# Performance work log

Hardware: AMD Instinct MI355X
Metric: run time of the kernel (lower is better)

The kernel has to match this reference:

```python
import jax, jax.numpy as jnp
import numpy as np

N = 100000
LEAKY_SLOPE = 0.2


def gat_conv(x, W, att_src, att_dst, b, src, dst, num_nodes):
    """PyG-style GATConv (concat=True). x:[N,Fin], W:[Fin,H*C], att_*:[1,H,C], b:[H*C]."""
    H, C = att_src.shape[1], att_src.shape[2]
    h = (x @ W).reshape(num_nodes, H, C)                      # [N,H,C]
    a_src = jnp.sum(h * att_src, axis=-1)                     # [N,H]
    a_dst = jnp.sum(h * att_dst, axis=-1)                     # [N,H]
    e = jax.nn.leaky_relu(a_src[src] + a_dst[dst], LEAKY_SLOPE)  # [E,H]
    # segment softmax over destination neighborhoods
    m = jax.ops.segment_max(e, dst, num_segments=num_nodes)   # [N,H]
    m = jnp.where(jnp.isfinite(m), m, 0.0)
    ex = jnp.exp(e - m[dst])                                  # [E,H]
    s = jax.ops.segment_sum(ex, dst, num_segments=num_nodes)  # [N,H]
    alpha = ex / (s[dst] + 1e-16)                             # [E,H]
    msg = h[src] * alpha[:, :, None]                          # [E,H,C]
    out = jax.ops.segment_sum(msg, dst, num_segments=num_nodes)  # [N,H,C]
    return out.reshape(num_nodes, H * C) + b


def setup_inputs() -> dict:
    key = jax.random.key(0)
    ks = jax.random.split(key, 8)
    F_in, H, C, n_cls = 256, 4, 32, 16
    E = 1_600_000
    x = jax.random.normal(ks[0], (N, F_in), dtype=jnp.float32)
    edge_index = jax.random.randint(ks[1], (2, E), 0, N, dtype=jnp.int64)
    sc1 = 1.0 / np.sqrt(F_in)
    sc2 = 1.0 / np.sqrt(H * C)
    return {
        "x": x,
        "edge_index": edge_index,
        "W1": jax.random.normal(ks[2], (F_in, H * C), dtype=jnp.float32) * sc1,
        "att_src1": jax.random.normal(ks[3], (1, H, C), dtype=jnp.float32) * sc2,
        "att_dst1": jax.random.normal(ks[4], (1, H, C), dtype=jnp.float32) * sc2,
        "b1": jnp.zeros((H * C,), dtype=jnp.float32),
        "W2": jax.random.normal(ks[5], (H * C, n_cls), dtype=jnp.float32) * sc2,
        "att_src2": jax.random.normal(ks[6], (1, 1, n_cls), dtype=jnp.float32) * 0.25,
        "att_dst2": jax.random.normal(ks[7], (1, 1, n_cls), dtype=jnp.float32) * 0.25,
        "b2": jnp.zeros((n_cls,), dtype=jnp.float32),
    }


def reference(x, edge_index, W1, att_src1, att_dst1, b1, W2, att_src2, att_dst2, b2):
    # add self-loops (PyG GATConv default)
    loop = jnp.arange(N, dtype=edge_index.dtype)
    src = jnp.concatenate([edge_index[0], loop])
    dst = jnp.concatenate([edge_index[1], loop])
    # eval mode: dropout(p=0.6) is identity
    h = gat_conv(x, W1, att_src1, att_dst1, b1, src, dst, N)
    h = jax.nn.elu(h)
    out = gat_conv(h, W2, att_src2, att_dst2, b2, src, dst, N)
    return out
```

## Files before the change

### kernel.cpp

```cpp
#include <hip/hip_runtime.h>
#include <hip/hip_fp16.h>
#include <cfloat>
#include <cmath>

#define LEAKY 0.2f

typedef _Float16 half8 __attribute__((ext_vector_type(8)));
typedef float f32x4 __attribute__((ext_vector_type(4)));

__device__ __forceinline__ void edge_sd(const int* __restrict__ ei, int e, int E, int& s, int& d) {
    if (e < E) { s = ei[e]; d = ei[E + e]; }
    else       { s = e - E; d = e - E; }
}

__global__ void hist_k(const int* __restrict__ ei, int E, int ET,
                       int* __restrict__ cnt, int* __restrict__ rank) {
    int e = blockIdx.x * 256 + threadIdx.x;
    if (e >= ET) return;
    int d = (e < E) ? ei[E + e] : e - E;
    rank[e] = atomicAdd(&cnt[d], 1);
}

__device__ __forceinline__ int wave_incl_scan(int x, int lane) {
#pragma unroll
    for (int off = 1; off < 64; off <<= 1) {
        int y = __shfl_up(x, off);
        if (lane >= off) x += y;
    }
    return x;
}

__global__ __launch_bounds__(1024) void scan_blk_k(const int* __restrict__ cnt,
                                                   int* __restrict__ rowptr,
                                                   int* __restrict__ part, int Nn) {
    __shared__ int wsum[16];
    const int t = threadIdx.x, lane = t & 63, w = t >> 6;
    const int i = blockIdx.x * 1024 + t;
    int v = (i < Nn) ? cnt[i] : 0;
    int sc = wave_incl_scan(v, lane);
    if (lane == 63) wsum[w] = sc;
    __syncthreads();
    if (w == 0 && lane < 16) {
        int x = wsum[lane];
#pragma unroll
        for (int off = 1; off < 16; off <<= 1) {
            int y = __shfl_up(x, off);
            if (lane >= off) x += y;
        }
        wsum[lane] = x;
    }
    __syncthreads();
    int excl = sc - v + (w ? wsum[w - 1] : 0);
    if (i < Nn) rowptr[i] = excl;
    if (t == 1023) part[blockIdx.x] = wsum[15];
}

__global__ __launch_bounds__(128) void scan_part_k(int* __restrict__ part, int nb) {
    __shared__ int sm[128];
    int t = threadIdx.x;
    int v = (t < nb) ? part[t] : 0;
    sm[t] = v; __syncthreads();
    for (int off = 1; off < 128; off <<= 1) {
        int add = (t >= off) ? sm[t - off] : 0;
        __syncthreads();
        sm[t] += add;
        __syncthreads();
    }
    if (t < nb) part[t] = sm[t] - v;
}

__global__ __launch_bounds__(1024) void scan_add_k(int* __restrict__ rowptr,
                                                   const int* __restrict__ part,
                                                   int Nn, int ET) {
    int i = blockIdx.x * 1024 + threadIdx.x;
    if (i < Nn) rowptr[i] += part[blockIdx.x];
    if (i == 0) rowptr[Nn] = ET;
}

__global__ void scatter_k(const int* __restrict__ ei, int E, int ET,
                          const int* __restrict__ rowptr, const int* __restrict__ rank,
                          int* __restrict__ srcs) {
    int e = blockIdx.x * 256 + threadIdx.x;
    if (e >= ET) return;
    int s, d; edge_sd(ei, e, E, s, d);
    srcs[rowptr[d] + rank[e]] = s;
}

__global__ void wpack1_k(const float* __restrict__ W1, _Float16* __restrict__ Wpk) {
    int g = blockIdx.x * 256 + threadIdx.x;
    if (g >= 4096) return;
    int t = g >> 9, s = (g >> 6) & 7, l = g & 63;
    int krow = s * 32 + ((l >> 4) << 3);
    int col = t * 16 + (l & 15);
    half8 v;
#pragma unroll
    for (int j = 0; j < 8; ++j) v[j] = (_Float16)W1[(size_t)(krow + j) * 128 + col];
    *(half8*)&Wpk[(size_t)g * 8] = v;
}

__global__ __launch_bounds__(512) void gemm1_k(const float* __restrict__ x,
                                               const _Float16* __restrict__ Wpk,
                                               _Float16* __restrict__ h1, int Mt) {
    __shared__ __align__(16) _Float16 xs[32 * 256];
    const int t = threadIdx.x;
    const int l = t & 63;
    const int w = t >> 6;
    const int mstr = w >> 2;
    const int npair = w & 3;

    half8 bf0[8], bf1[8];
#pragma unroll
    for (int s = 0; s < 8; ++s) {
        bf0[s] = *(const half8*)&Wpk[(size_t)(((npair * 2 + 0) * 8 + s) * 64 + l) * 8];
        bf1[s] = *(const half8*)&Wpk[(size_t)(((npair * 2 + 1) * 8 + s) * 64 + l) * 8];
    }

    const int r = t >> 4;
    const int kc = t & 15;
    const int swz = (r & 7) << 4;
    const int arow = mstr * 16 + (l & 15);
    const int aswz = (arow & 7) << 4;
    const int abase = arow * 256;

    for (int mt = blockIdx.x; mt < Mt; mt += gridDim.x) {
        const int mBase = mt * 32;
        const float4* xrow = (const float4*)(x + (size_t)(mBase + r) * 256);
#pragma unroll
        for (int i = 0; i < 4; ++i) {
            float4 v = xrow[kc + i * 16];
            union { _Float16 h[4]; uint2 u; } cv;
            cv.h[0] = (_Float16)v.x; cv.h[1] = (_Float16)v.y;
            cv.h[2] = (_Float16)v.z; cv.h[3] = (_Float16)v.w;
            int kb = kc * 8 + i * 128;
            *(uint2*)&xs[r * 256 + ((kb ^ swz) >> 1)] = cv.u;
        }
        __syncthreads();
        f32x4 acc0 = {0.f, 0.f, 0.f, 0.f}, acc1 = {0.f, 0.f, 0.f, 0.f};
#pragma unroll
        for (int s = 0; s < 8; ++s) {
            int kb = s * 64 + ((l >> 4) << 4);
            half8 a = *(const half8*)&xs[abase + ((kb ^ aswz) >> 1)];
            acc0 = __builtin_amdgcn_mfma_f32_16x16x32_f16(a, bf0[s], acc0, 0, 0, 0);
            acc1 = __builtin_amdgcn_mfma_f32_16x16x32_f16(a, bf1[s], acc1, 0, 0, 0);
        }
        const int drow = mBase + mstr * 16 + ((l >> 4) << 2);
        const int dcol = npair * 32 + (l & 15);
#pragma unroll
        for (int rr = 0; rr < 4; ++rr) {
            h1[(size_t)(drow + rr) * 128 + dcol]      = (_Float16)acc0[rr];
            h1[(size_t)(drow + rr) * 128 + dcol + 16] = (_Float16)acc1[rr];
        }
        __syncthreads();
    }
}

__global__ void acoef1_k(const __half* __restrict__ h1, const float* __restrict__ att_s,
                         const float* __restrict__ att_d, float* __restrict__ a1s,
                         float* __restrict__ a1d, int Nn) {
    int g = blockIdx.x * 256 + threadIdx.x;
    if (g >= Nn * 4) return;
    int node = g >> 2, head = g & 3;
    const __half2* hp = (const __half2*)(h1 + (size_t)node * 128 + head * 32);
    const float* as = att_s + head * 32;
    const float* ad = att_d + head * 32;
    float s = 0.0f, d = 0.0f;
#pragma unroll
    for (int c = 0; c < 16; ++c) {
        float2 v = __half22float2(hp[c]);
        s += v.x * as[2 * c] + v.y * as[2 * c + 1];
        d += v.x * ad[2 * c] + v.y * ad[2 * c + 1];
    }
    a1s[g] = s; a1d[g] = d;
}

__global__ __launch_bounds__(256) void agg1_k(const int* __restrict__ rowptr,
                                              const int* __restrict__ srcs,
                                              const float* __restrict__ a1s,
                                              const float* __restrict__ a1d,
                                              const __half* __restrict__ h1,
                                              const float* __restrict__ b1,
                                              const float* __restrict__ W2,
                                              const float* __restrict__ att_s2,
                                              const float* __restrict__ att_d2,
                                              __half* __restrict__ h2,
                                              float* __restrict__ a2s,
                                              float* __restrict__ a2d, int Nn) {
    __shared__ int   s_s[4][64];
    __shared__ float s_al[4][64][4];
    __shared__ float rowb[4][128];
    __shared__ float w2s[128 * 16];
    const int wv = threadIdx.x >> 6;
    const int lane = threadIdx.x & 63;
    const int n = blockIdx.x * 4 + wv;

    for (int i4 = threadIdx.x; i4 < 512; i4 += 256)
        *(float4*)&w2s[i4 * 4] = *(const float4*)&W2[i4 * 4];

    if (n < Nn) {
        const int beg = rowptr[n], end = rowptr[n + 1];
        const int cnt = end - beg;
        const float4 ad4 = ((const float4*)a1d)[n];

        int e = beg + lane;
        bool val = e < end;
        int sv = val ? srcs[e] : 0;
        float4 a = ((const float4*)a1s)[sv];
        float v0 = a.x + ad4.x, v1 = a.y + ad4.y, v2 = a.z + ad4.z, v3 = a.w + ad4.w;
        v0 = fmaxf(v0, LEAKY * v0); v1 = fmaxf(v1, LEAKY * v1);
        v2 = fmaxf(v2, LEAKY * v2); v3 = fmaxf(v3, LEAKY * v3);
        float al0 = val ? __expf(v0) : 0.0f, al1 = val ? __expf(v1) : 0.0f;
        float al2 = val ? __expf(v2) : 0.0f, al3 = val ? __expf(v3) : 0.0f;
        float t0 = al0, t1 = al1, t2 = al2, t3 = al3;
        for (int base = beg + 64; base < end; base += 64) {
            int ee = base + lane; bool vv = ee < end;
            int ss = vv ? srcs[ee] : 0;
            float4 aa = ((const float4*)a1s)[ss];
            float w0 = aa.x + ad4.x, w1 = aa.y + ad4.y, w2v = aa.z + ad4.z, w3 = aa.w + ad4.w;
            w0 = fmaxf(w0, LEAKY * w0); w1 = fmaxf(w1, LEAKY * w1);
            w2v = fmaxf(w2v, LEAKY * w2v); w3 = fmaxf(w3, LEAKY * w3);
            if (vv) { t0 += __expf(w0); t1 += __expf(w1); t2 += __expf(w2v); t3 += __expf(w3); }
        }
#pragma unroll
        for (int off = 1; off < 64; off <<= 1) {
            t0 += __shfl_xor(t0, off); t1 += __shfl_xor(t1, off);
            t2 += __shfl_xor(t2, off); t3 += __shfl_xor(t3, off);
        }
        const float i0 = 1.0f / (t0 + 1e-16f), i1 = 1.0f / (t1 + 1e-16f);
        const float i2 = 1.0f / (t2 + 1e-16f), i3 = 1.0f / (t3 + 1e-16f);

        const int hc = lane >> 4;
        float2 acc = make_float2(0.0f, 0.0f);
        const size_t lo = 2 * lane;

        s_s[wv][lane] = sv;
        s_al[wv][lane][0] = al0 * i0; s_al[wv][lane][1] = al1 * i1;
        s_al[wv][lane][2] = al2 * i2; s_al[wv][lane][3] = al3 * i3;
        int wcnt = cnt < 64 ? cnt : 64;
        int ko = 0;
        for (; ko + 4 <= wcnt; ko += 4) {
            int s0 = s_s[wv][ko+0], s1 = s_s[wv][ko+1];
            int s2 = s_s[wv][ko+2], s3 = s_s[wv][ko+3];
            float p0 = s_al[wv][ko+0][hc], p1 = s_al[wv][ko+1][hc];
            float p2 = s_al[wv][ko+2][hc], p3 = s_al[wv][ko+3][hc];
            float2 g0 = __half22float2(*(const __half2*)&h1[(size_t)s0 * 128 + lo]);
            float2 g1 = __half22float2(*(const __half2*)&h1[(size_t)s1 * 128 + lo]);
            float2 g2 = __half22float2(*(const __half2*)&h1[(size_t)s2 * 128 + lo]);
            float2 g3 = __half22float2(*(const __half2*)&h1[(size_t)s3 * 128 + lo]);
            acc.x = fmaf(p0, g0.x, acc.x); acc.y = fmaf(p0, g0.y, acc.y);
            acc.x = fmaf(p1, g1.x, acc.x); acc.y = fmaf(p1, g1.y, acc.y);
            acc.x = fmaf(p2, g2.x, acc.x); acc.y = fmaf(p2, g2.y, acc.y);
            acc.x = fmaf(p3, g3.x, acc.x); acc.y = fmaf(p3, g3.y, acc.y);
        }
        for (; ko < wcnt; ++ko) {
            int s = s_s[wv][ko];
            float p = s_al[wv][ko][hc];
            float2 g = __half22float2(*(const __half2*)&h1[(size_t)s * 128 + lo]);
            acc.x = fmaf(p, g.x, acc.x); acc.y = fmaf(p, g.y, acc.y);
        }
        for (int base = beg + 64; base < end; base += 64) {
            int ee = base + lane; bool vv = ee < end;
            int ss = vv ? srcs[ee] : 0;
            float4 aa = ((const float4*)a1s)[ss];
            float w0 = aa.x + ad4.x, w1 = aa.y + ad4.y, w2v = aa.z + ad4.z, w3 = aa.w + ad4.w;
            w0 = fmaxf(w0, LEAKY * w0); w1 = fmaxf(w1, LEAKY * w1);
            w2v = fmaxf(w2v, LEAKY * w2v); w3 = fmaxf(w3, LEAKY * w3);
            s_s[wv][lane] = ss;
            s_al[wv][lane][0] = vv ? __expf(w0) * i0 : 0.0f;
            s_al[wv][lane][1] = vv ? __expf(w1) * i1 : 0.0f;
            s_al[wv][lane][2] = vv ? __expf(w2v) * i2 : 0.0f;
            s_al[wv][lane][3] = vv ? __expf(w3) * i3 : 0.0f;
            int wc = end - base; if (wc > 64) wc = 64;
            for (int k2 = 0; k2 < wc; ++k2) {
                int s = s_s[wv][k2];
                float p = s_al[wv][k2][hc];
                float2 g = __half22float2(*(const __half2*)&h1[(size_t)s * 128 + lo]);
                acc.x = fmaf(p, g.x, acc.x); acc.y = fmaf(p, g.y, acc.y);
            }
        }
        float2 bb = *(const float2*)&b1[2 * lane];
        float ox = acc.x + bb.x, oy = acc.y + bb.y;
        ox = ox > 0.0f ? ox : expm1f(ox);
        oy = oy > 0.0f ? oy : expm1f(oy);
        rowb[wv][2 * lane] = ox;
        rowb[wv][2 * lane + 1] = oy;
    }
    __syncthreads();
    if (n >= Nn) return;

    const int q = lane >> 4, j = lane & 15;
    const float* rb = rowb[wv];
    float part = 0.0f;
#pragma unroll
    for (int kk = 0; kk < 32; ++kk) {
        int k = kk * 4 + q;
        part = fmaf(rb[k], w2s[k * 16 + j], part);
    }
    part += __shfl_xor(part, 16);
    part += __shfl_xor(part, 32);
    float vs = part * att_s2[j];
    float vd = part * att_d2[j];
#pragma unroll
    for (int off = 1; off < 16; off <<= 1) {
        vs += __shfl_xor(vs, off);
        vd += __shfl_xor(vd, off);
    }
    if (lane < 16) h2[(size_t)n * 16 + j] = __float2half(part);
    if (lane == 0) { a2s[n] = vs; a2d[n] = vd; }
}

__global__ __launch_bounds__(256) void agg2_k(const int* __restrict__ rowptr,
                                              const int* __restrict__ srcs,
                                              const float* __restrict__ a2s,
                                              const float* __restrict__ a2d,
                                              const __half* __restrict__ h2,
                                              const float* __restrict__ b2,
                                              float* __restrict__ dout, int Nn) {
    __shared__ int   s_s[4][64];
    __shared__ float s_al[4][64];
    const int wv = threadIdx.x >> 6;
    const int lane = threadIdx.x & 63;
    const int n = blockIdx.x * 4 + wv;
    if (n >= Nn) return;
    const int beg = rowptr[n], end = rowptr[n + 1];
    const int cnt = end - beg;
    const float adn = a2d[n];

    int e = beg + lane;
    bool val = e < end;
    int sv = val ? srcs[e] : 0;
    float av = a2s[sv] + adn;
    av = fmaxf(av, LEAKY * av);
    float al = val ? __expf(av) : 0.0f;
    float ss = al;
    for (int base = beg + 64; base < end; base += 64) {
        int ee = base + lane; bool vv = ee < end;
        float aw = a2s[vv ? srcs[ee] : 0] + adn;
        aw = fmaxf(aw, LEAKY * aw);
        if (vv) ss += __expf(aw);
    }
#pragma unroll
    for (int off = 1; off < 64; off <<= 1) ss += __shfl_xor(ss, off);
    const float sinv = 1.0f / (ss + 1e-16f);

    const int eg = lane >> 4, j = lane & 15;
    float acc = 0.0f;
    s_s[wv][lane] = sv;
    s_al[wv][lane] = al * sinv;
    int wcnt = cnt < 64 ? cnt : 64;
    int ko = eg;
    for (; ko + 4 < wcnt; ko += 8) {
        int s0 = s_s[wv][ko], s1 = s_s[wv][ko + 4];
        float p0 = s_al[wv][ko], p1 = s_al[wv][ko + 4];
        float g0 = __half2float(h2[(size_t)s0 * 16 + j]);
        float g1 = __half2float(h2[(size_t)s1 * 16 + j]);
        acc = fmaf(p0, g0, acc);
        acc = fmaf(p1, g1, acc);
    }
    for (; ko < wcnt; ko += 4) {
        acc = fmaf(s_al[wv][ko], __half2float(h2[(size_t)s_s[wv][ko] * 16 + j]), acc);
    }
    for (int base = beg + 64; base < end; base += 64) {
        int ee = base + lane; bool vv = ee < end;
        int sn = vv ? srcs[ee] : 0;
        float aw = a2s[sn] + adn;
        aw = fmaxf(aw, LEAKY * aw);
        s_s[wv][lane] = sn;
        s_al[wv][lane] = vv ? __expf(aw) * sinv : 0.0f;
        int wc = end - base; if (wc > 64) wc = 64;
        for (int k2 = eg; k2 < wc; k2 += 4) {
            acc = fmaf(s_al[wv][k2], __half2float(h2[(size_t)s_s[wv][k2] * 16 + j]), acc);
        }
    }
    acc += __shfl_xor(acc, 16);
    acc += __shfl_xor(acc, 32);
    if (lane < 16) dout[(size_t)n * 16 + j] = acc + b2[j];
}

extern "C" void kernel_launch(void* const* d_in, const int* in_sizes, int n_in,
                              void* d_out, int out_size, void* d_ws, size_t ws_size,
                              hipStream_t stream) {
    const float* x      = (const float*)d_in[0];
    const int*   ei     = (const int*)d_in[1];
    const float* W1     = (const float*)d_in[2];
    const float* att_s1 = (const float*)d_in[3];
    const float* att_d1 = (const float*)d_in[4];
    const float* b1     = (const float*)d_in[5];
    const float* W2     = (const float*)d_in[6];
    const float* att_s2 = (const float*)d_in[7];
    const float* att_d2 = (const float*)d_in[8];
    const float* b2     = (const float*)d_in[9];
    float* dout = (float*)d_out;

    const int Nn = in_sizes[0] / 256;
    const int E  = in_sizes[1] / 2;
    const int ET = E + Nn;

    char* p = (char*)d_ws;
    auto alloc = [&](size_t bytes) { char* r = p; p += (bytes + 255) & ~(size_t)255; return r; };
    _Float16* h1  = (_Float16*)alloc((size_t)Nn * 128 * 2);
    __half* h2    = (__half*)alloc((size_t)Nn * 16 * 2);
    _Float16* Wpk = (_Float16*)alloc(4096 * 8 * 2);
    float* a1s    = (float*)alloc((size_t)Nn * 4 * 4);
    float* a1d    = (float*)alloc((size_t)Nn * 4 * 4);
    float* a2s    = (float*)alloc((size_t)Nn * 4);
    float* a2d    = (float*)alloc((size_t)Nn * 4);
    int* rowptr   = (int*)alloc((size_t)(Nn + 1) * 4);
    int* cnt      = (int*)alloc((size_t)Nn * 4);
    int* rank     = (int*)alloc((size_t)ET * 4);
    int* part     = (int*)alloc(128 * 4);
    int* srcs     = (int*)alloc((size_t)ET * 4);

    const int nbScan = (Nn + 1023) / 1024;

    hipMemsetAsync(cnt, 0, (size_t)Nn * 4, stream);
    hist_k<<<dim3((ET + 255) / 256), dim3(256), 0, stream>>>(ei, E, ET, cnt, rank);
    scan_blk_k<<<dim3(nbScan), dim3(1024), 0, stream>>>(cnt, rowptr, part, Nn);
    scan_part_k<<<dim3(1), dim3(128), 0, stream>>>(part, nbScan);
    scan_add_k<<<dim3(nbScan), dim3(1024), 0, stream>>>(rowptr, part, Nn, ET);
    scatter_k<<<dim3((ET + 255) / 256), dim3(256), 0, stream>>>(ei, E, ET, rowptr, rank, srcs);
    wpack1_k<<<dim3(16), dim3(256), 0, stream>>>(W1, Wpk);
    gemm1_k<<<dim3(512), dim3(512), 0, stream>>>(x, Wpk, h1, Nn / 32);
    acoef1_k<<<dim3((Nn * 4 + 255) / 256), dim3(256), 0, stream>>>((const __half*)h1, att_s1, att_d1, a1s, a1d, Nn);
    agg1_k<<<dim3((Nn + 3) / 4), dim3(256), 0, stream>>>(rowptr, srcs, a1s, a1d,
                                                         (const __half*)h1, b1,
                                                         W2, att_s2, att_d2,
                                                         h2, a2s, a2d, Nn);
    agg2_k<<<dim3((Nn + 3) / 4), dim3(256), 0, stream>>>(rowptr, srcs, a2s, a2d, h2, b2, dout, Nn);
}
```

Baseline: 290.1 us.

## Fuse attention coefficient computation into GEMM epilogue and vectorize CSR build kernels

Removes the separate acoef1 kernel by computing per-head source and destination attention dot products in the GEMM epilogue. Each 16-lane group reduces its columns with xor shuffles and one lane writes the result. The histogram and scatter kernels now process four edges per thread with int4 loads, cutting thread count and improving load width. This assumes E is divisible by 4 and 16-byte alignment of the edge arrays, and the attention coefficients now come from fp32 accumulators rather than fp16-rounded h1.

```diff
diff --git a/kernel.cpp b/kernel.cpp
--- a/kernel.cpp
+++ b/kernel.cpp
@@ -13,12 +13,22 @@
     else       { s = e - E; d = e - E; }
 }
 
-__global__ void hist_k(const int* __restrict__ ei, int E, int ET,
+__global__ void hist_k(const int* __restrict__ ei, int E, int Nn,
                        int* __restrict__ cnt, int* __restrict__ rank) {
-    int e = blockIdx.x * 256 + threadIdx.x;
-    if (e >= ET) return;
-    int d = (e < E) ? ei[E + e] : e - E;
-    rank[e] = atomicAdd(&cnt[d], 1);
+    const int E4 = E >> 2;
+    int tid = blockIdx.x * 256 + threadIdx.x;
+    if (tid < E4) {
+        int4 d4 = *(const int4*)&ei[E + tid * 4];
+        int4 r;
+        r.x = atomicAdd(&cnt[d4.x], 1);
+        r.y = atomicAdd(&cnt[d4.y], 1);
+        r.z = atomicAdd(&cnt[d4.z], 1);
+        r.w = atomicAdd(&cnt[d4.w], 1);
+        *(int4*)&rank[tid * 4] = r;
+    } else {
+        int i = tid - E4;
+        if (i < Nn) rank[E + i] = atomicAdd(&cnt[i], 1);
+    }
 }
 
 __device__ __forceinline__ int wave_incl_scan(int x, int lane) {
@@ -77,13 +87,23 @@
     if (i == 0) rowptr[Nn] = ET;
 }
 
-__global__ void scatter_k(const int* __restrict__ ei, int E, int ET,
+__global__ void scatter_k(const int* __restrict__ ei, int E, int Nn,
                           const int* __restrict__ rowptr, const int* __restrict__ rank,
                           int* __restrict__ srcs) {
-    int e = blockIdx.x * 256 + threadIdx.x;
-    if (e >= ET) return;
-    int s, d; edge_sd(ei, e, E, s, d);
-    srcs[rowptr[d] + rank[e]] = s;
+    const int E4 = E >> 2;
+    int tid = blockIdx.x * 256 + threadIdx.x;
+    if (tid < E4) {
+        int4 s4 = *(const int4*)&ei[tid * 4];
+        int4 d4 = *(const int4*)&ei[E + tid * 4];
+        int4 r4 = *(const int4*)&rank[tid * 4];
+        srcs[rowptr[d4.x] + r4.x] = s4.x;
+        srcs[rowptr[d4.y] + r4.y] = s4.y;
+        srcs[rowptr[d4.z] + r4.z] = s4.z;
+        srcs[rowptr[d4.w] + r4.w] = s4.w;
+    } else {
+        int i = tid - E4;
+        if (i < Nn) srcs[rowptr[i] + rank[E + i]] = i;
+    }
 }
 
 __global__ void wpack1_k(const float* __restrict__ W1, _Float16* __restrict__ Wpk) {
@@ -100,7 +120,11 @@
 
 __global__ __launch_bounds__(512) void gemm1_k(const float* __restrict__ x,
                                                const _Float16* __restrict__ Wpk,
-                                               _Float16* __restrict__ h1, int Mt) {
+                                               const float* __restrict__ att_s,
+                                               const float* __restrict__ att_d,
+                                               _Float16* __restrict__ h1,
+                                               float* __restrict__ a1s,
+                                               float* __restrict__ a1d, int Mt) {
     __shared__ __align__(16) _Float16 xs[32 * 256];
     const int t = threadIdx.x;
     const int l = t & 63;
@@ -114,6 +138,10 @@
         bf0[s] = *(const half8*)&Wpk[(size_t)(((npair * 2 + 0) * 8 + s) * 64 + l) * 8];
         bf1[s] = *(const half8*)&Wpk[(size_t)(((npair * 2 + 1) * 8 + s) * 64 + l) * 8];
     }
+    const float as0 = att_s[npair * 32 + (l & 15)];
+    const float as1 = att_s[npair * 32 + 16 + (l & 15)];
+    const float ad0 = att_d[npair * 32 + (l & 15)];
+    const float ad1 = att_d[npair * 32 + 16 + (l & 15)];
 
     const int r = t >> 4;
     const int kc = t & 15;
@@ -149,28 +177,20 @@
         for (int rr = 0; rr < 4; ++rr) {
             h1[(size_t)(drow + rr) * 128 + dcol]      = (_Float16)acc0[rr];
             h1[(size_t)(drow + rr) * 128 + dcol + 16] = (_Float16)acc1[rr];
+            float ps = acc0[rr] * as0 + acc1[rr] * as1;
+            float pd = acc0[rr] * ad0 + acc1[rr] * ad1;
+#pragma unroll
+            for (int off = 1; off < 16; off <<= 1) {
+                ps += __shfl_xor(ps, off);
+                pd += __shfl_xor(pd, off);
+            }
+            if ((l & 15) == 0) {
+                a1s[(drow + rr) * 4 + npair] = ps;
+                a1d[(drow + rr) * 4 + npair] = pd;
+            }
         }
         __syncthreads();
     }
-}
-
-__global__ void acoef1_k(const __half* __restrict__ h1, const float* __restrict__ att_s,
-                         const float* __restrict__ att_d, float* __restrict__ a1s,
-                         float* __restrict__ a1d, int Nn) {
-    int g = blockIdx.x * 256 + threadIdx.x;
-    if (g >= Nn * 4) return;
-    int node = g >> 2, head = g & 3;
-    const __half2* hp = (const __half2*)(h1 + (size_t)node * 128 + head * 32);
-    const float* as = att_s + head * 32;
-    const float* ad = att_d + head * 32;
-    float s = 0.0f, d = 0.0f;
-#pragma unroll
-    for (int c = 0; c < 16; ++c) {
-        float2 v = __half22float2(hp[c]);
-        s += v.x * as[2 * c] + v.y * as[2 * c + 1];
-        d += v.x * ad[2 * c] + v.y * ad[2 * c + 1];
-    }
-    a1s[g] = s; a1d[g] = d;
 }
 
 __global__ __launch_bounds__(256) void agg1_k(const int* __restrict__ rowptr,
@@ -411,16 +431,16 @@
     int* srcs     = (int*)alloc((size_t)ET * 4);
 
     const int nbScan = (Nn + 1023) / 1024;
+    const int nBuild = (E / 4 + Nn + 255) / 256;
 
     hipMemsetAsync(cnt, 0, (size_t)Nn * 4, stream);
-    hist_k<<<dim3((ET + 255) / 256), dim3(256), 0, stream>>>(ei, E, ET, cnt, rank);
+    wpack1_k<<<dim3(16), dim3(256), 0, stream>>>(W1, Wpk);
+    hist_k<<<dim3(nBuild), dim3(256), 0, stream>>>(ei, E, Nn, cnt, rank);
     scan_blk_k<<<dim3(nbScan), dim3(1024), 0, stream>>>(cnt, rowptr, part, Nn);
     scan_part_k<<<dim3(1), dim3(128), 0, stream>>>(part, nbScan);
     scan_add_k<<<dim3(nbScan), dim3(1024), 0, stream>>>(rowptr, part, Nn, ET);
-    scatter_k<<<dim3((ET + 255) / 256), dim3(256), 0, stream>>>(ei, E, ET, rowptr, rank, srcs);
-    wpack1_k<<<dim3(16), dim3(256), 0, stream>>>(W1, Wpk);
-    gemm1_k<<<dim3(512), dim3(512), 0, stream>>>(x, Wpk, h1, Nn / 32);
-    acoef1_k<<<dim3((Nn * 4 + 255) / 256), dim3(256), 0, stream>>>((const __half*)h1, att_s1, att_d1, a1s, a1d, Nn);
+    scatter_k<<<dim3(nBuild), dim3(256), 0, stream>>>(ei, E, Nn, rowptr, rank, srcs);
+    gemm1_k<<<dim3(512), dim3(512), 0, stream>>>(x, Wpk, att_s1, att_d1, h1, a1s, a1d, Nn / 32);
     agg1_k<<<dim3((Nn + 3) / 4), dim3(256), 0, stream>>>(rowptr, srcs, a1s, a1d,
                                                          (const __half*)h1, b1,
                                                          W2, att_s2, att_d2,
```

New measurement: 280.2 us. 1.04x faster.
